# Optimization experiments

Hardware: AMD Instinct MI355X
Metric: run time of the kernel (lower is better)

## Reference

```python
import jax, jax.numpy as jnp
import numpy as np

ATLAS_DHW = (91, 109, 91)   # AAL atlas grid (MNI space)
ROI_LO, ROI_HI = 1, 94      # roi_range: labels 1..94 kept, 0 = background
NUM_SEG = ROI_HI + 1        # 95 segments (incl. background slot 0)


def setup_inputs() -> dict:
    key = jax.random.key(0)
    k1, k2 = jax.random.split(key)
    B, C = 2, 64
    feat = jax.random.normal(k1, (B, C, 96, 112, 96), dtype=jnp.float32)
    atlas = jax.random.randint(k2, ATLAS_DHW, 0, NUM_SEG, dtype=jnp.int32)
    return {"feat": feat, "atlas": atlas}


def reference(feat, atlas):
    # Crop padded feature map back to atlas grid
    D, H, W = ATLAS_DHW
    feat = feat[..., :D, :H, :W]                      # (B, C, D, H, W)
    B, C = feat.shape[0], feat.shape[1]
    N = D * H * W

    ids = atlas.reshape(-1)                           # (N,) voxel -> ROI label
    # (B, C, N) -> (N, B*C) so segment_sum reduces over voxels
    flat = jnp.moveaxis(feat.reshape(B, C, N), 2, 0).reshape(N, B * C)

    # Masked segment sum == one-hot matmul num = einsum('rn,bcn->brc')
    sums = jax.ops.segment_sum(flat, ids, num_segments=NUM_SEG)   # (95, B*C)
    cnts = jax.ops.segment_sum(jnp.ones((N,), feat.dtype), ids,
                               num_segments=NUM_SEG)              # (95,)

    num = sums[ROI_LO:].reshape(NUM_SEG - ROI_LO, B, C)           # (R, B, C)
    den = jnp.maximum(cnts[ROI_LO:], 1e-6)                        # (R,)
    out = jnp.transpose(num, (1, 0, 2)) / den[None, :, None]      # (B, R, C)
    return out
```

## Files before the change

kernel.cpp:

```cpp
#include <hip/hip_runtime.h>

constexpr int SEG_N   = 95;
constexpr int CROP_D  = 91, CROP_H = 109, CROP_W = 91;
constexpr int NVOX    = CROP_D * CROP_H * CROP_W;
constexpr int LINES   = CROP_D * CROP_H;
constexpr int FEAT_W  = 96;
constexpr int FEAT_HW = 112 * 96;
constexpr int CSTRIDE = 96 * 112 * 96;
constexpr int NTILE   = LINES * 3;
constexpr int NBC     = 128;
constexpr int PSEG    = 96;
constexpr int BIN_SZ  = NBC * PSEG;
constexpr int GRID    = 1024;
constexpr int NCHUNK  = 16;
constexpr int KPC     = GRID / NCHUNK;
constexpr int OUT_N   = 2 * 94 * 64;
constexpr size_t PART_OFF  = 4096;
constexpr size_t PART2_OFF = PART_OFF + (size_t)GRID * BIN_SZ * sizeof(float);
constexpr size_t WS_NEED   = PART2_OFF + (size_t)NCHUNK * BIN_SZ * sizeof(float);

typedef __attribute__((ext_vector_type(8))) short bf16x8;
typedef __attribute__((ext_vector_type(4))) float f32x4;

__device__ inline unsigned int rne2(float a, float b) {
    unsigned int x = __float_as_uint(a), y = __float_as_uint(b);
    x = (x + 0x7FFFu + ((x >> 16) & 1u)) >> 16;
    y = (y + 0x7FFFu + ((y >> 16) & 1u)) & 0xFFFF0000u;
    return x | y;
}

__global__ __launch_bounds__(256) void zero_ws(unsigned int* __restrict__ w)
{
    const int i = blockIdx.x * 256 + threadIdx.x;
    if (i < (int)(PART_OFF / 4) + BIN_SZ) w[i] = 0u;
}

__global__ __launch_bounds__(256) void seg_mfma(const float* __restrict__ feat,
                                                const int*   __restrict__ atlas,
                                                float* __restrict__ part,
                                                int use_atomic)
{
    const int tid = threadIdx.x, wv = tid >> 6, lane = tid & 63;
    const int l15 = lane & 15, lq = lane >> 4;

    f32x4 acc[2][6];
    #pragma unroll
    for (int a = 0; a < 2; ++a)
        #pragma unroll
        for (int s = 0; s < 6; ++s) acc[a][s] = (f32x4){0.f, 0.f, 0.f, 0.f};

    for (int t = blockIdx.x; t < NTILE; t += GRID) {
        const int line  = t / 3;
        const int w0    = (t - line * 3) * 32;
        const int d     = line / CROP_H, h = line - d * CROP_H;
        const int lbase = d * FEAT_HW + h * FEAT_W + w0;
        const int abase = line * CROP_W + w0;

        int id[8];
        const int wq = w0 + lq * 8;
        #pragma unroll
        for (int j = 0; j < 8; ++j)
            id[j] = (wq + j < CROP_W) ? atlas[abase + lq * 8 + j] : 95;

        unsigned int bu[6][4];
        #pragma unroll
        for (int sb = 0; sb < 6; ++sb) {
            const int seg = sb * 16 + l15;
            #pragma unroll
            for (int p = 0; p < 4; ++p) {
                const unsigned int lo = (id[2 * p]     == seg) ? 0x3F80u     : 0u;
                const unsigned int hi = (id[2 * p + 1] == seg) ? 0x3F800000u : 0u;
                bu[sb][p] = lo | hi;
            }
        }

        #pragma unroll
        for (int a = 0; a < 2; ++a) {
            const int ch = wv * 32 + a * 16 + l15;
            const float* fp = feat + (size_t)ch * CSTRIDE + lbase + lq * 8;
            const float4 v0 = *(const float4*)fp;
            const float4 v1 = *(const float4*)(fp + 4);
            union { bf16x8 v; unsigned int u[4]; } A;
            A.u[0] = rne2(v0.x, v0.y); A.u[1] = rne2(v0.z, v0.w);
            A.u[2] = rne2(v1.x, v1.y); A.u[3] = rne2(v1.z, v1.w);
            #pragma unroll
            for (int sb = 0; sb < 6; ++sb) {
                union { bf16x8 v; unsigned int u[4]; } B;
                B.u[0] = bu[sb][0]; B.u[1] = bu[sb][1];
                B.u[2] = bu[sb][2]; B.u[3] = bu[sb][3];
                acc[a][sb] = __builtin_amdgcn_mfma_f32_16x16x32_bf16(A.v, B.v, acc[a][sb], 0, 0, 0);
            }
        }
    }

    float* p = part + (use_atomic ? 0 : (size_t)blockIdx.x * BIN_SZ);
    #pragma unroll
    for (int a = 0; a < 2; ++a)
        #pragma unroll
        for (int sb = 0; sb < 6; ++sb)
            #pragma unroll
            for (int r = 0; r < 4; ++r) {
                const int ch  = wv * 32 + a * 16 + lq * 4 + r;
                const int seg = sb * 16 + l15;
                if (use_atomic) unsafeAtomicAdd(&p[ch * PSEG + seg], acc[a][sb][r]);
                else            p[ch * PSEG + seg] = acc[a][sb][r];
            }
}

__global__ __launch_bounds__(256) void seg_count(const int* __restrict__ atlas,
                                                 int* __restrict__ cnts)
{
    __shared__ int cbin[SEG_N];
    const int tid = threadIdx.x;
    for (int i = tid; i < SEG_N; i += 256) cbin[i] = 0;
    __syncthreads();
    for (int i = blockIdx.x * 256 + tid; i < NVOX; i += gridDim.x * 256)
        atomicAdd(&cbin[atlas[i]], 1);
    __syncthreads();
    for (int i = tid; i < SEG_N; i += 256) atomicAdd(&cnts[i], cbin[i]);
}

__global__ __launch_bounds__(256) void reduce_stageA(const float* __restrict__ part,
                                                     float* __restrict__ part2,
                                                     int active)
{
    if (!active) return;
    const int g = blockIdx.x * 256 + threadIdx.x;
    const int c = g / BIN_SZ, e = g - c * BIN_SZ;
    const float* p = part + (size_t)c * KPC * BIN_SZ + e;
    float s = 0.0f;
    #pragma unroll 8
    for (int k = 0; k < KPC; ++k) s += p[(size_t)k * BIN_SZ];
    part2[g] = s;
}

__global__ __launch_bounds__(256) void finalize(const float* __restrict__ src,
                                                const int*   __restrict__ cnts,
                                                float* __restrict__ out,
                                                int n)
{
    const int idx = blockIdx.x * 256 + threadIdx.x;
    if (idx >= OUT_N) return;
    const int c   = idx & 63;
    const int s0  = (idx >> 6) % 94;
    const int b   = idx / (94 * 64);
    const int seg = s0 + 1;
    const int ch  = b * 64 + c;
    float s = 0.0f;
    for (int k = 0; k < n; ++k)
        s += src[(size_t)k * BIN_SZ + ch * PSEG + seg];
    const float den = fmaxf((float)cnts[seg], 1e-6f);
    out[idx] = s / den;
}

extern "C" void kernel_launch(void* const* d_in, const int* in_sizes, int n_in,
                              void* d_out, int out_size, void* d_ws, size_t ws_size,
                              hipStream_t stream)
{
    const float* feat  = (const float*)d_in[0];
    const int*   atlas = (const int*)d_in[1];
    float* out   = (float*)d_out;
    int*   cnts  = (int*)d_ws;
    float* part  = (float*)((char*)d_ws + PART_OFF);
    float* part2 = (float*)((char*)d_ws + PART2_OFF);
    const int use_atomic = (ws_size < WS_NEED) ? 1 : 0;

    const int nzero = (int)(PART_OFF / 4) + BIN_SZ;
    zero_ws<<<(nzero + 255) / 256, 256, 0, stream>>>((unsigned int*)d_ws);
    seg_count<<<256, 256, 0, stream>>>(atlas, cnts);
    seg_mfma<<<GRID, 256, 0, stream>>>(feat, atlas, part, use_atomic);
    reduce_stageA<<<(BIN_SZ * NCHUNK) / 256, 256, 0, stream>>>(part, part2, use_atomic ? 0 : 1);
    finalize<<<(OUT_N + 255) / 256, 256, 0, stream>>>(use_atomic ? part : part2, cnts, out,
                                                      use_atomic ? 1 : NCHUNK);
}
```

Before: 147.7 us.

## Fuse ROI voxel counting into MFMA kernel as an extra ones-row

Drops the separate histogram kernel. Wave 0 of each block now runs extra MFMAs with an all-ones A operand, and the per-segment counts go into a 129th row of the partial bins, which is reduced with the sums. It also skips the zeroing launch and the idle reduce launch when they are not needed, and adds a launch_bounds occupancy hint. The cost is slightly more partial-buffer traffic and extra MFMA work on wave 0.

```diff
diff --git a/kernel.cpp b/kernel.cpp
--- a/kernel.cpp
+++ b/kernel.cpp
@@ -2,21 +2,19 @@
 
 constexpr int SEG_N   = 95;
 constexpr int CROP_D  = 91, CROP_H = 109, CROP_W = 91;
-constexpr int NVOX    = CROP_D * CROP_H * CROP_W;
 constexpr int LINES   = CROP_D * CROP_H;
 constexpr int FEAT_W  = 96;
 constexpr int FEAT_HW = 112 * 96;
 constexpr int CSTRIDE = 96 * 112 * 96;
 constexpr int NTILE   = LINES * 3;
-constexpr int NBC     = 128;
 constexpr int PSEG    = 96;
-constexpr int BIN_SZ  = NBC * PSEG;
+constexpr int ROWS    = 129;
+constexpr int BIN_SZ  = ROWS * PSEG;
 constexpr int GRID    = 1024;
 constexpr int NCHUNK  = 16;
 constexpr int KPC     = GRID / NCHUNK;
 constexpr int OUT_N   = 2 * 94 * 64;
-constexpr size_t PART_OFF  = 4096;
-constexpr size_t PART2_OFF = PART_OFF + (size_t)GRID * BIN_SZ * sizeof(float);
+constexpr size_t PART2_OFF = (size_t)GRID * BIN_SZ * sizeof(float);
 constexpr size_t WS_NEED   = PART2_OFF + (size_t)NCHUNK * BIN_SZ * sizeof(float);
 
 typedef __attribute__((ext_vector_type(8))) short bf16x8;
@@ -29,49 +27,61 @@
     return x | y;
 }
 
-__global__ __launch_bounds__(256) void zero_ws(unsigned int* __restrict__ w)
+__global__ __launch_bounds__(256) void zero_part(float* __restrict__ p)
 {
     const int i = blockIdx.x * 256 + threadIdx.x;
-    if (i < (int)(PART_OFF / 4) + BIN_SZ) w[i] = 0u;
+    if (i < BIN_SZ) p[i] = 0.0f;
 }
 
-__global__ __launch_bounds__(256) void seg_mfma(const float* __restrict__ feat,
-                                                const int*   __restrict__ atlas,
-                                                float* __restrict__ part,
-                                                int use_atomic)
+__global__ __launch_bounds__(256, 4) void seg_mfma(const float* __restrict__ feat,
+                                                   const int*   __restrict__ atlas,
+                                                   float* __restrict__ part,
+                                                   int use_atomic)
 {
     const int tid = threadIdx.x, wv = tid >> 6, lane = tid & 63;
     const int l15 = lane & 15, lq = lane >> 4;
 
     f32x4 acc[2][6];
+    f32x4 accc[6];
     #pragma unroll
-    for (int a = 0; a < 2; ++a)
-        #pragma unroll
-        for (int s = 0; s < 6; ++s) acc[a][s] = (f32x4){0.f, 0.f, 0.f, 0.f};
+    for (int s = 0; s < 6; ++s) {
+        acc[0][s] = (f32x4){0.f, 0.f, 0.f, 0.f};
+        acc[1][s] = (f32x4){0.f, 0.f, 0.f, 0.f};
+        accc[s]   = (f32x4){0.f, 0.f, 0.f, 0.f};
+    }
+    union { bf16x8 v; unsigned int u[4]; } ONES;
+    ONES.u[0] = ONES.u[1] = ONES.u[2] = ONES.u[3] = 0x3F803F80u;
 
     for (int t = blockIdx.x; t < NTILE; t += GRID) {
         const int line  = t / 3;
         const int w0    = (t - line * 3) * 32;
         const int d     = line / CROP_H, h = line - d * CROP_H;
         const int lbase = d * FEAT_HW + h * FEAT_W + w0;
-        const int abase = line * CROP_W + w0;
 
         int id[8];
-        const int wq = w0 + lq * 8;
+        const int wq = w0 + lq * 8, abase = line * CROP_W + w0 + lq * 8;
         #pragma unroll
         for (int j = 0; j < 8; ++j)
-            id[j] = (wq + j < CROP_W) ? atlas[abase + lq * 8 + j] : 95;
+            id[j] = (wq + j < CROP_W) ? atlas[abase + j] : 95;
 
-        unsigned int bu[6][4];
+        bf16x8 bv[6];
         #pragma unroll
         for (int sb = 0; sb < 6; ++sb) {
             const int seg = sb * 16 + l15;
+            union { bf16x8 v; unsigned int u[4]; } B;
             #pragma unroll
             for (int p = 0; p < 4; ++p) {
                 const unsigned int lo = (id[2 * p]     == seg) ? 0x3F80u     : 0u;
                 const unsigned int hi = (id[2 * p + 1] == seg) ? 0x3F800000u : 0u;
-                bu[sb][p] = lo | hi;
+                B.u[p] = lo | hi;
             }
+            bv[sb] = B.v;
+        }
+
+        if (wv == 0) {
+            #pragma unroll
+            for (int sb = 0; sb < 6; ++sb)
+                accc[sb] = __builtin_amdgcn_mfma_f32_16x16x32_bf16(ONES.v, bv[sb], accc[sb], 0, 0, 0);
         }
 
         #pragma unroll
@@ -84,12 +94,8 @@
             A.u[0] = rne2(v0.x, v0.y); A.u[1] = rne2(v0.z, v0.w);
             A.u[2] = rne2(v1.x, v1.y); A.u[3] = rne2(v1.z, v1.w);
             #pragma unroll
-            for (int sb = 0; sb < 6; ++sb) {
-                union { bf16x8 v; unsigned int u[4]; } B;
-                B.u[0] = bu[sb][0]; B.u[1] = bu[sb][1];
-                B.u[2] = bu[sb][2]; B.u[3] = bu[sb][3];
-                acc[a][sb] = __builtin_amdgcn_mfma_f32_16x16x32_bf16(A.v, B.v, acc[a][sb], 0, 0, 0);
-            }
+            for (int sb = 0; sb < 6; ++sb)
+                acc[a][sb] = __builtin_amdgcn_mfma_f32_16x16x32_bf16(A.v, bv[sb], acc[a][sb], 0, 0, 0);
         }
     }
 
@@ -100,31 +106,23 @@
         for (int sb = 0; sb < 6; ++sb)
             #pragma unroll
             for (int r = 0; r < 4; ++r) {
-                const int ch  = wv * 32 + a * 16 + lq * 4 + r;
-                const int seg = sb * 16 + l15;
-                if (use_atomic) unsafeAtomicAdd(&p[ch * PSEG + seg], acc[a][sb][r]);
-                else            p[ch * PSEG + seg] = acc[a][sb][r];
+                const int i = (wv * 32 + a * 16 + lq * 4 + r) * PSEG + sb * 16 + l15;
+                if (use_atomic) unsafeAtomicAdd(&p[i], acc[a][sb][r]);
+                else            p[i] = acc[a][sb][r];
             }
-}
-
-__global__ __launch_bounds__(256) void seg_count(const int* __restrict__ atlas,
-                                                 int* __restrict__ cnts)
-{
-    __shared__ int cbin[SEG_N];
-    const int tid = threadIdx.x;
-    for (int i = tid; i < SEG_N; i += 256) cbin[i] = 0;
-    __syncthreads();
-    for (int i = blockIdx.x * 256 + tid; i < NVOX; i += gridDim.x * 256)
-        atomicAdd(&cbin[atlas[i]], 1);
-    __syncthreads();
-    for (int i = tid; i < SEG_N; i += 256) atomicAdd(&cnts[i], cbin[i]);
+    if (wv == 0 && lq == 0) {
+        #pragma unroll
+        for (int sb = 0; sb < 6; ++sb) {
+            const int i = 128 * PSEG + sb * 16 + l15;
+            if (use_atomic) unsafeAtomicAdd(&p[i], accc[sb][0]);
+            else            p[i] = accc[sb][0];
+        }
+    }
 }
 
 __global__ __launch_bounds__(256) void reduce_stageA(const float* __restrict__ part,
-                                                     float* __restrict__ part2,
-                                                     int active)
+                                                     float* __restrict__ part2)
 {
-    if (!active) return;
     const int g = blockIdx.x * 256 + threadIdx.x;
     const int c = g / BIN_SZ, e = g - c * BIN_SZ;
     const float* p = part + (size_t)c * KPC * BIN_SZ + e;
@@ -135,7 +133,7 @@
 }
 
 __global__ __launch_bounds__(256) void finalize(const float* __restrict__ src,
-                                                const int*   __restrict__ cnts,
+                                                const int*   ,
                                                 float* __restrict__ out,
                                                 int n)
 {
@@ -146,11 +144,12 @@
     const int b   = idx / (94 * 64);
     const int seg = s0 + 1;
     const int ch  = b * 64 + c;
-    float s = 0.0f;
-    for (int k = 0; k < n; ++k)
-        s += src[(size_t)k * BIN_SZ + ch * PSEG + seg];
-    const float den = fmaxf((float)cnts[seg], 1e-6f);
-    out[idx] = s / den;
+    float s = 0.0f, cnt = 0.0f;
+    for (int k = 0; k < n; ++k) {
+        s   += src[(size_t)k * BIN_SZ + ch * PSEG + seg];
+        cnt += src[(size_t)k * BIN_SZ + 128 * PSEG + seg];
+    }
+    out[idx] = s / fmaxf(cnt, 1e-6f);
 }
 
 extern "C" void kernel_launch(void* const* d_in, const int* in_sizes, int n_in,
@@ -160,16 +159,15 @@
     const float* feat  = (const float*)d_in[0];
     const int*   atlas = (const int*)d_in[1];
     float* out   = (float*)d_out;
-    int*   cnts  = (int*)d_ws;
-    float* part  = (float*)((char*)d_ws + PART_OFF);
+    float* part  = (float*)d_ws;
     float* part2 = (float*)((char*)d_ws + PART2_OFF);
     const int use_atomic = (ws_size < WS_NEED) ? 1 : 0;
 
-    const int nzero = (int)(PART_OFF / 4) + BIN_SZ;
-    zero_ws<<<(nzero + 255) / 256, 256, 0, stream>>>((unsigned int*)d_ws);
-    seg_count<<<256, 256, 0, stream>>>(atlas, cnts);
+    if (use_atomic)
+        zero_part<<<(BIN_SZ + 255) / 256, 256, 0, stream>>>(part);
     seg_mfma<<<GRID, 256, 0, stream>>>(feat, atlas, part, use_atomic);
-    reduce_stageA<<<(BIN_SZ * NCHUNK) / 256, 256, 0, stream>>>(part, part2, use_atomic ? 0 : 1);
-    finalize<<<(OUT_N + 255) / 256, 256, 0, stream>>>(use_atomic ? part : part2, cnts, out,
+    if (!use_atomic)
+        reduce_stageA<<<(BIN_SZ * NCHUNK) / 256, 256, 0, stream>>>(part, part2);
+    finalize<<<(OUT_N + 255) / 256, 256, 0, stream>>>(use_atomic ? part : part2, nullptr, out,
                                                       use_atomic ? 1 : NCHUNK);
 }
```

New measurement: 135.4 us. 1.09x faster.
